# Kernel optimization log

Measured on AMD Instinct MI355X. Metric: run time of the kernel, lower is better.

The kernel has to match this reference:

```python
import jax, jax.numpy as jnp
import numpy as np

CUTOFF = 5.0
BOX = 20.0
EPS = 1e-5


def _neighbor_list_np(cutoff, coords, cell):
    # coords: [N,3] float32, cell: [3,3]. Returns (pair_first, pair_second, pair_image)
    inv_cell = np.linalg.inv(cell)
    proj = coords @ inv_cell
    frac = np.fmod(proj, 1.0)                      # matches torch.fmod (sign-preserving)
    woff = np.floor(proj).astype(np.int64)          # torch.div(..., rounding_mode='floor')
    wrapped = (frac @ cell).astype(coords.dtype)
    inv_lengths = np.linalg.norm(inv_cell, axis=0)
    nb = (np.floor(cutoff * inv_lengths + EPS) + 1).astype(np.int64)
    ranges = [np.arange(-int(n), int(n) + 1) for n in nb]
    # image grid ordered (i1 outer, i2, i3 inner) to match the nested torch loops
    images = np.stack(np.meshgrid(*ranges, indexing='ij'), axis=-1).reshape(-1, 3)
    off_cart = images.astype(coords.dtype) @ cell   # [K,3]
    drij = wrapped[:, None, :] - wrapped[None, :, :]           # [N,N,3]
    diff = drij[None, :, :, :] + off_cart[:, None, None, :]    # [K,N,N,3]
    dist = np.linalg.norm(diff, axis=-1)                       # [K,N,N]
    mask = dist < cutoff
    zero_k = int(np.where((images == 0).all(axis=1))[0][0])
    np.fill_diagonal(mask[zero_k], False)                      # drop self pairs in home image
    k, i, j = np.nonzero(mask)  # row-major (k,i,j) == per-image blocks of (i,j), same order as torch
    woff_ij = woff[i] - woff[j]
    pair_image = images[k] - woff_ij
    return i, j, pair_image


def setup_inputs() -> dict:
    key = jax.random.key(0)
    n_mol, n_at = 16, 512
    coordinates = jax.random.uniform(key, (n_mol, n_at, 3), dtype=jnp.float32) * BOX
    nonblank = jnp.ones((n_mol, n_at), dtype=bool)
    real_atoms = jnp.arange(n_mol * n_at, dtype=jnp.int32)
    inv_real_atoms = jnp.arange(n_mol * n_at, dtype=jnp.int32)
    cell = jnp.tile((BOX * jnp.eye(3, dtype=jnp.float32))[None], (n_mol, 1, 1))
    mol_index = jnp.arange(n_mol * n_at, dtype=jnp.int32) // n_at
    return dict(coordinates=coordinates, nonblank=nonblank, real_atoms=real_atoms,
                inv_real_atoms=inv_real_atoms, cell=cell, mol_index=mol_index,
                n_molecules=n_mol, n_atoms_max=n_at)


def reference(coordinates, nonblank, real_atoms, inv_real_atoms, cell, mol_index,
              n_molecules, n_atoms_max):
    # --- neighbor-list construction (torch.no_grad section): host numpy, vectorized over images ---
    coords_np = np.asarray(coordinates)
    cell_np = np.asarray(cell)
    nb_np = np.asarray(nonblank)
    pfs, pss, ofs = [], [], []
    for m in range(n_molecules):
        r = coords_np[m][nb_np[m]]
        pf, ps, of = _neighbor_list_np(CUTOFF, r, cell_np[m])
        if len(pf) == 0:
            continue
        pfs.append(pf + m * n_atoms_max)
        pss.append(ps + m * n_atoms_max)
        ofs.append(of)
    pf = np.concatenate(pfs)
    ps = np.concatenate(pss)
    of = np.concatenate(ofs)
    n_images = max(1, int(np.abs(of).max()))

    pair_first = inv_real_atoms[jnp.asarray(pf)]
    pair_second = inv_real_atoms[jnp.asarray(ps)]
    offsets = jnp.asarray(of.astype(np.int32))
    n_off = 2 * n_images + 1
    o1, o2, o3 = (offsets + n_images).T
    offset_index = o3 + n_off * (o2 + n_off * o1)
    pair_mol = mol_index[pair_first]
    pair_cell = cell[pair_mol]                                   # [P,3,3]
    pair_offsets = jnp.einsum('pk,pkl->pl', offsets.astype(cell.dtype), pair_cell)

    # --- differentiable distance evaluation ---
    coordflat = coordinates.reshape(n_molecules * n_atoms_max, 3)[real_atoms]
    paircoord = coordflat[pair_first] - coordflat[pair_second] + pair_offsets
    distflat2 = jnp.linalg.norm(paircoord, axis=1)
    return distflat2, pair_first, pair_second, paircoord, offsets, offset_index
```

## Files before the change

### kernel.cpp

```cpp
#include <hip/hip_runtime.h>

#define NMOL 16
#define NAT  512
#define NK   27

#define SSMAX 24.999998092651367f

__device__ __forceinline__ float wrap1(float v) {
    return __fmul_rn(__fmul_rn(v, 0.05f), 20.0f);
}

__device__ __forceinline__ int probe_code(float wx, float wy, float wz,
                                          float wjx, float wjy, float wjz,
                                          bool self) {
    float dx = __fsub_rn(wx, wjx);
    float dy = __fsub_rn(wy, wjy);
    float dz = __fsub_rn(wz, wjz);
    int ox = (dx > 15.0f) ? -1 : ((dx < -15.0f) ? 1 : 0);
    int oy = (dy > 15.0f) ? -1 : ((dy < -15.0f) ? 1 : 0);
    int oz = (dz > 15.0f) ? -1 : ((dz < -15.0f) ? 1 : 0);
    float ax = __fadd_rn(dx, 20.0f * (float)ox);
    float ay = __fadd_rn(dy, 20.0f * (float)oy);
    float az = __fadd_rn(dz, 20.0f * (float)oz);
    float ss = __fadd_rn(__fadd_rn(__fmul_rn(ax, ax), __fmul_rn(ay, ay)),
                         __fmul_rn(az, az));
    bool hit = (ss < SSMAX) && !self;
    return hit ? ((ox + 1) * 9 + (oy + 1) * 3 + (oz + 1)) : 31;
}

__global__ __launch_bounds__(256, 8) void pass_count(const float* __restrict__ coords,
                                                     int* __restrict__ cnt,
                                                     int* __restrict__ blkmol) {
    __shared__ float rr[NAT * 3];
    __shared__ int cur[2][4][NK];
    const int blk  = blockIdx.x;
    const int m    = blk >> 6;
    const int g0   = (blk & 63) * 2;
    const int t    = threadIdx.x;
    const int w    = t >> 6;
    const int lane = t & 63;
    const int iA   = g0 * 4 + w;
    const int iB   = iA + 4;

    const float4* cm4 = reinterpret_cast<const float4*>(coords + (size_t)m * NAT * 3);
    float4* rr4 = reinterpret_cast<float4*>(rr);
    rr4[t] = cm4[t];
    if (t < 128) rr4[t + 256] = cm4[t + 256];
    if (t < 2 * 4 * NK) ((int*)cur)[t] = 0;
    __syncthreads();

    const float wAx = wrap1(rr[iA * 3 + 0]), wAy = wrap1(rr[iA * 3 + 1]), wAz = wrap1(rr[iA * 3 + 2]);
    const float wBx = wrap1(rr[iB * 3 + 0]), wBy = wrap1(rr[iB * 3 + 1]), wBz = wrap1(rr[iB * 3 + 2]);

    #pragma unroll
    for (int it = 0; it < NAT / 64; ++it) {
        const int j = it * 64 + lane;
        float wjx = wrap1(rr[j * 3 + 0]);
        float wjy = wrap1(rr[j * 3 + 1]);
        float wjz = wrap1(rr[j * 3 + 2]);
        int cA = probe_code(wAx, wAy, wAz, wjx, wjy, wjz, j == iA);
        int cB = probe_code(wBx, wBy, wBz, wjx, wjy, wjz, j == iB);
        if (cA != 31) atomicAdd(&cur[0][w][cA], 1);
        if (cB != 31) atomicAdd(&cur[1][w][cB], 1);
    }
    __syncthreads();
    if (t < 216) {
        int uu = t / 108, rem = t % 108, ww = rem / 27, k = rem % 27;
        int i = (g0 + uu) * 4 + ww;
        cnt[(m * NK + k) * NAT + i] = cur[uu][ww][k];
    }
    if (w == 0) {
        int s = 0;
        #pragma unroll
        for (int x = lane; x < 216; x += 64) s += ((int*)cur)[x];
        #pragma unroll
        for (int d = 1; d < 64; d <<= 1) s += __shfl_xor(s, d, 64);
        if (lane == 0) blkmol[blk] = s;
    }
}

__global__ __launch_bounds__(1024, 4) void scan_emit(const float* __restrict__ coords,
                                                     const int* __restrict__ cnt,
                                                     const int* __restrict__ blkmol,
                                                     float* __restrict__ out, int P) {
    __shared__ float rr[NAT * 3];
    __shared__ int scnt[NK * NAT];
    __shared__ int ctot[NK];
    __shared__ int cexcl[NK];
    __shared__ int tls[NMOL];

    const int blk  = blockIdx.x;
    const int m    = blk >> 4;
    const int q    = blk & 15;
    const int t    = threadIdx.x;
    const int w    = t >> 6;
    const int lane = t & 63;

    const float4* cm4 = reinterpret_cast<const float4*>(coords + (size_t)m * NAT * 3);
    float4* rr4 = reinterpret_cast<float4*>(rr);
    if (t < 384) rr4[t] = cm4[t];

    const int* cslice = cnt + m * NK * NAT;
    for (int x = t; x < NK * NAT; x += 1024) scnt[x] = cslice[x];

    {
        int v = blkmol[t];
        #pragma unroll
        for (int d = 1; d < 64; d <<= 1) v += __shfl_xor(v, d, 64);
        if (lane == 0) tls[w] = v;
    }
    __syncthreads();

    for (int k = w; k < NK; k += 16) {
        int* ck = scnt + k * NAT;
        int v[8];
        int tot = 0;
        #pragma unroll
        for (int e = 0; e < 8; ++e) { v[e] = ck[lane * 8 + e]; tot += v[e]; }
        int incl = tot;
        #pragma unroll
        for (int d = 1; d < 64; d <<= 1) {
            int u = __shfl_up(incl, d, 64);
            if (lane >= d) incl += u;
        }
        int acc = incl - tot;
        #pragma unroll
        for (int e = 0; e < 8; ++e) { int tmp = v[e]; ck[lane * 8 + e] = acc; acc += tmp; }
        if (lane == 63) ctot[k] = incl;
    }
    __syncthreads();
    if (t == 0) {
        int run = 0;
        for (int mm = 0; mm < m; ++mm) run += tls[mm];
        for (int k = 0; k < NK; ++k) { cexcl[k] = run; run += ctot[k]; }
    }
    __syncthreads();
    for (int x = t; x < NK * NAT; x += 1024) scnt[x] += cexcl[x >> 9];
    __syncthreads();

    const unsigned long long ltmask =
        (lane == 0) ? 0ull : (~0ull >> (64 - lane));

    #pragma unroll
    for (int u = 0; u < 2; ++u) {
        const int i  = q * 32 + 2 * w + u;
        const float rx = rr[i*3+0], ry = rr[i*3+1], rz = rr[i*3+2];
        const float wx = wrap1(rx), wy = wrap1(ry), wz = wrap1(rz);
        const int pf = m * NAT + i;

        #pragma unroll
        for (int it = 0; it < NAT / 64; ++it) {
            const int j = it * 64 + lane;
            const float rjx = rr[j*3+0], rjy = rr[j*3+1], rjz = rr[j*3+2];
            int code = probe_code(wx, wy, wz,
                                  wrap1(rjx), wrap1(rjy), wrap1(rjz), j == i);
            bool hit = (code != 31);
            int kk = hit ? code : 0;

            unsigned long long grp = __ballot(hit);
            #pragma unroll
            for (int b = 0; b < 5; ++b) {
                unsigned long long bm = __ballot((kk >> b) & 1);
                grp &= ((kk >> b) & 1) ? bm : ~bm;
            }
            int leader = hit ? (__ffsll((unsigned long long)grp) - 1) : 0;
            int cntg   = __popcll(grp);
            int rank   = __popcll(grp & ltmask);

            int base = 0;
            if (hit && lane == leader)
                base = atomicAdd(&scnt[kk * NAT + i], cntg);
            base = __shfl(base, leader, 64);

            if (hit) {
                int p = base + rank;
                if (p < P) {
                    int ox = kk / 9;
                    int rem = kk - ox * 9;
                    int oy = rem / 3;
                    int oz = rem - oy * 3;
                    ox -= 1; oy -= 1; oz -= 1;
                    float cx = 20.0f * (float)ox;
                    float cy = 20.0f * (float)oy;
                    float cz = 20.0f * (float)oz;
                    float px = __fadd_rn(__fsub_rn(rx, rjx), cx);
                    float py = __fadd_rn(__fsub_rn(ry, rjy), cy);
                    float pz = __fadd_rn(__fsub_rn(rz, rjz), cz);
                    float ss = __fadd_rn(__fadd_rn(__fmul_rn(px, px), __fmul_rn(py, py)),
                                         __fmul_rn(pz, pz));
                    out[p]                 = __fsqrt_rn(ss);
                    out[P + p]             = (float)pf;
                    out[2 * P + p]         = (float)(m * NAT + j);
                    out[3 * P + 3 * p + 0] = px;
                    out[3 * P + 3 * p + 1] = py;
                    out[3 * P + 3 * p + 2] = pz;
                    out[6 * P + 3 * p + 0] = (float)ox;
                    out[6 * P + 3 * p + 1] = (float)oy;
                    out[6 * P + 3 * p + 2] = (float)oz;
                    out[9 * P + p]         = (float)kk;
                }
            }
        }
    }
}

extern "C" void kernel_launch(void* const* d_in, const int* in_sizes, int n_in,
                              void* d_out, int out_size, void* d_ws, size_t ws_size,
                              hipStream_t stream) {
    (void)in_sizes; (void)n_in; (void)ws_size;
    const float* coords = (const float*)d_in[0];
    int* cnt    = (int*)d_ws;
    int* blkmol = cnt + NMOL * NK * NAT;
    float* out  = (float*)d_out;
    const int P = out_size / 10;

    hipLaunchKernelGGL(pass_count, dim3(NMOL * NAT / 8), dim3(256), 0, stream,
                       coords, cnt, blkmol);
    hipLaunchKernelGGL(scan_emit, dim3(256), dim3(1024), 0, stream,
                       coords, cnt, blkmol, out, P);
}
```

Baseline: 99.13 us.

## Replace per-molecule scan_emit with hierarchical per-block-strip scan and emit

The count pass now also writes per-block, per-image subtotals. The emit kernel becomes 1024 small blocks of 256 threads, matching the count pass layout. Each block derives its write offsets from a 64-wide scan of those subtotals plus a short local prefix over its own 8-atom strip. Before, each of 256 blocks loaded and scanned the full 27x512 count table in shared memory, and that redundant load-and-scan work is gone. The change also cuts shared memory use, which should raise occupancy, at the cost of a small extra workspace array and more scattered small global reads.

```diff
diff --git a/kernel.cpp b/kernel.cpp
--- a/kernel.cpp
+++ b/kernel.cpp
@@ -30,12 +30,14 @@
 
 __global__ __launch_bounds__(256, 8) void pass_count(const float* __restrict__ coords,
                                                      int* __restrict__ cnt,
+                                                     int* __restrict__ sub,
                                                      int* __restrict__ blkmol) {
     __shared__ float rr[NAT * 3];
     __shared__ int cur[2][4][NK];
     const int blk  = blockIdx.x;
     const int m    = blk >> 6;
-    const int g0   = (blk & 63) * 2;
+    const int b    = blk & 63;
+    const int g0   = b * 2;
     const int t    = threadIdx.x;
     const int w    = t >> 6;
     const int lane = t & 63;
@@ -69,6 +71,14 @@
         int i = (g0 + uu) * 4 + ww;
         cnt[(m * NK + k) * NAT + i] = cur[uu][ww][k];
     }
+    if (t < NK) {
+        int s = 0;
+        #pragma unroll
+        for (int uu = 0; uu < 2; ++uu)
+            #pragma unroll
+            for (int ww = 0; ww < 4; ++ww) s += cur[uu][ww][t];
+        sub[(m * NK + t) * 64 + b] = s;
+    }
     if (w == 0) {
         int s = 0;
         #pragma unroll
@@ -79,89 +89,99 @@
     }
 }
 
-__global__ __launch_bounds__(1024, 4) void scan_emit(const float* __restrict__ coords,
-                                                     const int* __restrict__ cnt,
-                                                     const int* __restrict__ blkmol,
-                                                     float* __restrict__ out, int P) {
+__global__ __launch_bounds__(256, 8) void pass_emit(const float* __restrict__ coords,
+                                                    const int* __restrict__ cnt,
+                                                    const int* __restrict__ sub,
+                                                    const int* __restrict__ blkmol,
+                                                    float* __restrict__ out, int P) {
     __shared__ float rr[NAT * 3];
-    __shared__ int scnt[NK * NAT];
-    __shared__ int ctot[NK];
-    __shared__ int cexcl[NK];
+    __shared__ int cur[2][4][NK];
+    __shared__ int strip[8][NK];
+    __shared__ int ctot[NK], cpre[NK], kexcl[NK];
     __shared__ int tls[NMOL];
-
     const int blk  = blockIdx.x;
-    const int m    = blk >> 4;
-    const int q    = blk & 15;
+    const int m    = blk >> 6;
+    const int b    = blk & 63;
+    const int g0   = b * 2;
     const int t    = threadIdx.x;
     const int w    = t >> 6;
     const int lane = t & 63;
 
     const float4* cm4 = reinterpret_cast<const float4*>(coords + (size_t)m * NAT * 3);
     float4* rr4 = reinterpret_cast<float4*>(rr);
-    if (t < 384) rr4[t] = cm4[t];
-
-    const int* cslice = cnt + m * NK * NAT;
-    for (int x = t; x < NK * NAT; x += 1024) scnt[x] = cslice[x];
-
-    {
-        int v = blkmol[t];
+    rr4[t] = cm4[t];
+    if (t < 128) rr4[t + 256] = cm4[t + 256];
+
+    for (int mm = w; mm < NMOL; mm += 4) {
+        int v = blkmol[mm * 64 + lane];
         #pragma unroll
         for (int d = 1; d < 64; d <<= 1) v += __shfl_xor(v, d, 64);
-        if (lane == 0) tls[w] = v;
-    }
-    __syncthreads();
-
-    for (int k = w; k < NK; k += 16) {
-        int* ck = scnt + k * NAT;
-        int v[8];
-        int tot = 0;
-        #pragma unroll
-        for (int e = 0; e < 8; ++e) { v[e] = ck[lane * 8 + e]; tot += v[e]; }
-        int incl = tot;
+        if (lane == 0) tls[mm] = v;
+    }
+    for (int k = w; k < NK; k += 4) {
+        int v = sub[(m * NK + k) * 64 + lane];
+        int incl = v;
         #pragma unroll
         for (int d = 1; d < 64; d <<= 1) {
             int u = __shfl_up(incl, d, 64);
             if (lane >= d) incl += u;
         }
-        int acc = incl - tot;
-        #pragma unroll
-        for (int e = 0; e < 8; ++e) { int tmp = v[e]; ck[lane * 8 + e] = acc; acc += tmp; }
-        if (lane == 63) ctot[k] = incl;
+        int tot   = __shfl(incl, 63, 64);
+        int exclb = __shfl(incl - v, b, 64);
+        if (lane == 0) { ctot[k] = tot; cpre[k] = exclb; }
+    }
+    if (t < 216) {
+        int uu = t / 108, rem = t % 108, ww = rem / 27, k = rem % 27;
+        int i = (g0 + uu) * 4 + ww;
+        strip[uu * 4 + ww][k] = cnt[(m * NK + k) * NAT + i];
     }
     __syncthreads();
     if (t == 0) {
         int run = 0;
         for (int mm = 0; mm < m; ++mm) run += tls[mm];
-        for (int k = 0; k < NK; ++k) { cexcl[k] = run; run += ctot[k]; }
-    }
-    __syncthreads();
-    for (int x = t; x < NK * NAT; x += 1024) scnt[x] += cexcl[x >> 9];
-    __syncthreads();
-
+        for (int k = 0; k < NK; ++k) { kexcl[k] = run; run += ctot[k]; }
+    }
+    __syncthreads();
+    if (t < 216) {
+        int uu = t / 108, rem = t % 108, ww = rem / 27, k = rem % 27;
+        int a = uu * 4 + ww;
+        int ip = 0;
+        for (int a2 = 0; a2 < a; ++a2) ip += strip[a2][k];
+        cur[uu][ww][k] = kexcl[k] + cpre[k] + ip;
+    }
+    __syncthreads();
+
+    const int iA = g0 * 4 + w, iB = iA + 4;
+    const float rAx = rr[iA * 3 + 0], rAy = rr[iA * 3 + 1], rAz = rr[iA * 3 + 2];
+    const float rBx = rr[iB * 3 + 0], rBy = rr[iB * 3 + 1], rBz = rr[iB * 3 + 2];
+    const float wAx = wrap1(rAx), wAy = wrap1(rAy), wAz = wrap1(rAz);
+    const float wBx = wrap1(rBx), wBy = wrap1(rBy), wBz = wrap1(rBz);
     const unsigned long long ltmask =
         (lane == 0) ? 0ull : (~0ull >> (64 - lane));
 
     #pragma unroll
-    for (int u = 0; u < 2; ++u) {
-        const int i  = q * 32 + 2 * w + u;
-        const float rx = rr[i*3+0], ry = rr[i*3+1], rz = rr[i*3+2];
-        const float wx = wrap1(rx), wy = wrap1(ry), wz = wrap1(rz);
-        const int pf = m * NAT + i;
-
-        #pragma unroll
-        for (int it = 0; it < NAT / 64; ++it) {
-            const int j = it * 64 + lane;
-            const float rjx = rr[j*3+0], rjy = rr[j*3+1], rjz = rr[j*3+2];
-            int code = probe_code(wx, wy, wz,
-                                  wrap1(rjx), wrap1(rjy), wrap1(rjz), j == i);
+    for (int it = 0; it < NAT / 64; ++it) {
+        const int j = it * 64 + lane;
+        const float rjx = rr[j * 3 + 0], rjy = rr[j * 3 + 1], rjz = rr[j * 3 + 2];
+        const float wjx = wrap1(rjx), wjy = wrap1(rjy), wjz = wrap1(rjz);
+
+        #pragma unroll
+        for (int uu = 0; uu < 2; ++uu) {
+            const int i  = (uu == 0) ? iA : iB;
+            const float rx = (uu == 0) ? rAx : rBx;
+            const float ry = (uu == 0) ? rAy : rBy;
+            const float rz = (uu == 0) ? rAz : rBz;
+            int code = (uu == 0)
+                ? probe_code(wAx, wAy, wAz, wjx, wjy, wjz, j == iA)
+                : probe_code(wBx, wBy, wBz, wjx, wjy, wjz, j == iB);
             bool hit = (code != 31);
             int kk = hit ? code : 0;
 
             unsigned long long grp = __ballot(hit);
             #pragma unroll
-            for (int b = 0; b < 5; ++b) {
-                unsigned long long bm = __ballot((kk >> b) & 1);
-                grp &= ((kk >> b) & 1) ? bm : ~bm;
+            for (int bb = 0; bb < 5; ++bb) {
+                unsigned long long bm = __ballot((kk >> bb) & 1);
+                grp &= ((kk >> bb) & 1) ? bm : ~bm;
             }
             int leader = hit ? (__ffsll((unsigned long long)grp) - 1) : 0;
             int cntg   = __popcll(grp);
@@ -169,7 +189,7 @@
 
             int base = 0;
             if (hit && lane == leader)
-                base = atomicAdd(&scnt[kk * NAT + i], cntg);
+                base = atomicAdd(&cur[uu][w][kk], cntg);
             base = __shfl(base, leader, 64);
 
             if (hit) {
@@ -189,7 +209,7 @@
                     float ss = __fadd_rn(__fadd_rn(__fmul_rn(px, px), __fmul_rn(py, py)),
                                          __fmul_rn(pz, pz));
                     out[p]                 = __fsqrt_rn(ss);
-                    out[P + p]             = (float)pf;
+                    out[P + p]             = (float)(m * NAT + i);
                     out[2 * P + p]         = (float)(m * NAT + j);
                     out[3 * P + 3 * p + 0] = px;
                     out[3 * P + 3 * p + 1] = py;
@@ -210,12 +230,13 @@
     (void)in_sizes; (void)n_in; (void)ws_size;
     const float* coords = (const float*)d_in[0];
     int* cnt    = (int*)d_ws;
-    int* blkmol = cnt + NMOL * NK * NAT;
+    int* sub    = cnt + NMOL * NK * NAT;
+    int* blkmol = sub + NMOL * NK * 64;
     float* out  = (float*)d_out;
     const int P = out_size / 10;
 
     hipLaunchKernelGGL(pass_count, dim3(NMOL * NAT / 8), dim3(256), 0, stream,
-                       coords, cnt, blkmol);
-    hipLaunchKernelGGL(scan_emit, dim3(256), dim3(1024), 0, stream,
-                       coords, cnt, blkmol, out, P);
-}
+                       coords, cnt, sub, blkmol);
+    hipLaunchKernelGGL(pass_emit, dim3(NMOL * NAT / 8), dim3(256), 0, stream,
+                       coords, cnt, sub, blkmol, out, P);
+}
```

New measurement: 100.9 us. No clear change (+1.7%).
